# Kernel tuning notes

Hardware: AMD Instinct MI355X
Metric: run time of the kernel (lower is better)

## Reference

```python
import jax, jax.numpy as jnp
import numpy as np

B, N, C, L = 32, 1024, 128, 4

def setup_inputs() -> dict:
    key = jax.random.key(0)
    ks = jax.random.split(key, 8)
    x = jax.random.normal(ks[0], (B, N, C), dtype=jnp.float32)
    # binary adjacency: nonzero entries become unit-weight edges (edge weights unused in module)
    adj = jax.random.randint(ks[1], (B, N, N), 0, 2).astype(jnp.float32)
    mask = jnp.ones((B, N), dtype=jnp.float32)
    s = 1.0 / np.sqrt(C)
    weight = jax.random.uniform(ks[2], (L, C, C), minval=-s, maxval=s, dtype=jnp.float32)
    w_ih = jax.random.uniform(ks[3], (L, 3 * C, C), minval=-s, maxval=s, dtype=jnp.float32)
    w_hh = jax.random.uniform(ks[4], (L, 3 * C, C), minval=-s, maxval=s, dtype=jnp.float32)
    b_ih = jax.random.uniform(ks[5], (L, 3 * C), minval=-s, maxval=s, dtype=jnp.float32)
    b_hh = jax.random.uniform(ks[6], (L, 3 * C), minval=-s, maxval=s, dtype=jnp.float32)
    return {"x": x, "adj": adj, "mask": mask, "weight": weight,
            "w_ih": w_ih, "w_hh": w_hh, "b_ih": b_ih, "b_hh": b_hh}

def _gru_cell(m, h, w_ih, w_hh, b_ih, b_hh):
    # PyTorch GRUCell, gate order (r, z, n)
    gx = m @ w_ih.T + b_ih
    gh = h @ w_hh.T + b_hh
    xr, xz, xn = jnp.split(gx, 3, axis=-1)
    hr, hz, hn = jnp.split(gh, 3, axis=-1)
    r = jax.nn.sigmoid(xr + hr)
    z = jax.nn.sigmoid(xz + hz)
    n = jnp.tanh(xn + r * hn)
    return (1.0 - z) * n + z * h

def reference(x, adj, mask, weight, w_ih, w_hh, b_ih, b_hh):
    h = x  # [B, N, C]; in_channels == out_channels so no zero-padding needed
    for i in range(L):
        hw = jnp.einsum('bnc,cd->bnd', h, weight[i])
        # scatter-add of messages source->target == A^T @ (h W), unit edge weights
        m = jnp.einsum('bjn,bjd->bnd', adj, hw)
        h = _gru_cell(m, h, w_ih[i], w_hh[i], b_ih[i], b_hh[i])
    return h * mask[:, :, None]
```

## Files before the change

kernel.cpp:

```cpp
#include <hip/hip_runtime.h>
#include <stdint.h>


#define NB 32
#define NN 1024
#define NC 128
#define NL 4
#define MTOT (NB * NN)

#define KT 64
#define PITCH 72
#define MP 136

typedef __attribute__((ext_vector_type(8))) short s16x8;
typedef __attribute__((ext_vector_type(4))) float f32x4;
typedef __attribute__((ext_vector_type(2))) unsigned int u32x2;
typedef unsigned short U16;
typedef unsigned int U32;

__device__ __forceinline__ U16 f2bf(float f) {
    union { float f; U32 u; } v; v.f = f;
    return (U16)((v.u + 0x7FFFu + ((v.u >> 16) & 1u)) >> 16);
}
__device__ __forceinline__ float bf2f(U16 h) {
    union { U32 u; float f; } v; v.u = ((U32)h) << 16;
    return v.f;
}
__device__ __forceinline__ void splitbf(float x, U16& hi, U16& lo) {
    hi = f2bf(x);
    lo = f2bf(x - bf2f(hi));
}
__device__ __forceinline__ float sigmoidf_(float x) { return 1.f / (1.f + __expf(-x)); }

__device__ __forceinline__ void glds16(const void* g, void* l) {
    __builtin_amdgcn_global_load_lds(
        (const __attribute__((address_space(1))) void*)g,
        (__attribute__((address_space(3))) void*)l, 16, 0, 0);
}

#define SWZ(row, g) ((row) * 64 + ((((g) ^ ((row) & 7))) * 8))

__global__ __launch_bounds__(256) void k_setup(
    const float* __restrict__ adj, U16* __restrict__ adjT,
    const float* __restrict__ w, const float* __restrict__ wih, const float* __restrict__ whh,
    U16* __restrict__ wThi, U16* __restrict__ wTlo,
    U16* __restrict__ wihhi, U16* __restrict__ wihlo,
    U16* __restrict__ whhhi, U16* __restrict__ whhlo,
    const float* __restrict__ x, U16* __restrict__ hhi, U16* __restrict__ hlo)
{
    __shared__ float t[64 * 65];
    const int bid = blockIdx.x, tid = threadIdx.x;
    if (bid < 8192) {
        const int b = bid >> 8, rem = bid & 255;
        const int j0 = (rem & 15) * 64, n0 = (rem >> 4) * 64;
        const int rr = tid >> 4, c4 = (tid & 15) * 4;
#pragma unroll
        for (int p = 0; p < 4; ++p) {
            int j = p * 16 + rr;
            f32x4 v = *(const f32x4*)&adj[((size_t)b << 20) + ((size_t)(j0 + j) << 10) + n0 + c4];
#pragma unroll
            for (int u = 0; u < 4; ++u) t[j * 65 + c4 + u] = v[u];
        }
        __syncthreads();
#pragma unroll
        for (int p = 0; p < 4; ++p) {
            int n = p * 16 + rr;
            U16 h0 = f2bf(t[(c4 + 0) * 65 + n]);
            U16 h1 = f2bf(t[(c4 + 1) * 65 + n]);
            U16 h2 = f2bf(t[(c4 + 2) * 65 + n]);
            U16 h3 = f2bf(t[(c4 + 3) * 65 + n]);
            u32x2 pk; pk[0] = (U32)h0 | ((U32)h1 << 16); pk[1] = (U32)h2 | ((U32)h3 << 16);
            *(u32x2*)&adjT[((size_t)b << 20) + ((size_t)(n0 + n) << 10) + j0 + c4] = pk;
        }
    } else if (bid < 9984) {
        int i = (bid - 8192) * 256 + tid;
        if (i < 65536) {
            int l = i >> 14, rem = i & 16383, c = rem >> 7, d = rem & 127;
            U16 hi, lo; splitbf(w[i], hi, lo);
            int o = (l << 14) + (d << 7) + c;
            wThi[o] = hi; wTlo[o] = lo;
        } else if (i < 262144) {
            int j = i - 65536;
            U16 hi, lo; splitbf(wih[j], hi, lo);
            wihhi[j] = hi; wihlo[j] = lo;
        } else {
            int j = i - 262144;
            U16 hi, lo; splitbf(whh[j], hi, lo);
            whhhi[j] = hi; whhlo[j] = lo;
        }
    } else {
        int base = (bid - 9984) * 2048 + tid;
#pragma unroll
        for (int p = 0; p < 8; ++p) {
            int i = base + p * 256;
            U16 hi, lo; splitbf(x[i], hi, lo);
            hhi[i] = hi; hlo[i] = lo;
        }
    }
}

struct __align__(16) Smem3 {
    union {
        struct { U16 A[2][128 * PITCH]; U16 B[2][128 * PITCH]; } s;
        float bounce[128 * 129];
    };
};

__global__ __launch_bounds__(256, 2) void k_hw(
    const U16* __restrict__ Ahi, const U16* __restrict__ Alo,
    const U16* __restrict__ Bhi, const U16* __restrict__ Blo,
    U16* __restrict__ Ohi, U16* __restrict__ Olo)
{
    __shared__ Smem3 sm;
    const int tid = threadIdx.x;
    const int lane = tid & 63, wv = tid >> 6;
    const int wr = (wv & 1) * 64, wc = (wv >> 1) * 64;
    const int lm = lane & 15, lk8 = (lane >> 4) * 8;
    const int m0 = blockIdx.x * 128;

    f32x4 acc[4][4] = {};

    for (int kc = 0; kc < 128; kc += KT) {
#pragma unroll
        for (int t = 0; t < 4; ++t) {
            int i = tid + t * 256; int r = i >> 3, v = (i & 7) * 8;
            *(s16x8*)&sm.s.A[0][r * PITCH + v] = *(const s16x8*)&Ahi[(size_t)(m0 + r) * 128 + kc + v];
            *(s16x8*)&sm.s.A[1][r * PITCH + v] = *(const s16x8*)&Alo[(size_t)(m0 + r) * 128 + kc + v];
        }
#pragma unroll
        for (int t = 0; t < 4; ++t) {
            int i = tid + t * 256; int r = i >> 3, v = (i & 7) * 8;
            *(s16x8*)&sm.s.B[0][r * PITCH + v] = *(const s16x8*)&Bhi[r * 128 + kc + v];
            *(s16x8*)&sm.s.B[1][r * PITCH + v] = *(const s16x8*)&Blo[r * 128 + kc + v];
        }
        __syncthreads();
#pragma unroll
        for (int ks = 0; ks < 2; ++ks) {
            const int ko = ks * 32 + lk8;
            s16x8 ahi[4], alo[4], bhi[4], blo[4];
#pragma unroll
            for (int q = 0; q < 4; ++q) {
                ahi[q] = *(const s16x8*)&sm.s.A[0][(wr + q * 16 + lm) * PITCH + ko];
                alo[q] = *(const s16x8*)&sm.s.A[1][(wr + q * 16 + lm) * PITCH + ko];
                bhi[q] = *(const s16x8*)&sm.s.B[0][(wc + q * 16 + lm) * PITCH + ko];
                blo[q] = *(const s16x8*)&sm.s.B[1][(wc + q * 16 + lm) * PITCH + ko];
            }
#pragma unroll
            for (int rt = 0; rt < 4; ++rt)
#pragma unroll
                for (int ct = 0; ct < 4; ++ct) {
                    f32x4 a = acc[rt][ct];
                    a = __builtin_amdgcn_mfma_f32_16x16x32_bf16(ahi[rt], bhi[ct], a, 0, 0, 0);
                    a = __builtin_amdgcn_mfma_f32_16x16x32_bf16(ahi[rt], blo[ct], a, 0, 0, 0);
                    a = __builtin_amdgcn_mfma_f32_16x16x32_bf16(alo[rt], bhi[ct], a, 0, 0, 0);
                    acc[rt][ct] = a;
                }
        }
        __syncthreads();
    }
#pragma unroll
    for (int rt = 0; rt < 4; ++rt)
#pragma unroll
        for (int ct = 0; ct < 4; ++ct)
#pragma unroll
            for (int r = 0; r < 4; ++r)
                sm.bounce[(wr + rt * 16 + (lane >> 4) * 4 + r) * 129 + wc + ct * 16 + lm] = acc[rt][ct][r];
    __syncthreads();
    const int b = m0 >> 10, j0 = m0 & 1023;
    for (int t = 0; t < 32; ++t) {
        int i = tid + t * 256; int d = i >> 6, j2 = (i & 63) * 2;
        float x0 = sm.bounce[j2 * 129 + d], x1 = sm.bounce[(j2 + 1) * 129 + d];
        U16 h0, l0, h1, l1; splitbf(x0, h0, l0); splitbf(x1, h1, l1);
        size_t o = (((size_t)(b * 128 + d)) << 10) + j0 + j2;
        *(U32*)&Ohi[o] = (U32)h0 | ((U32)h1 << 16);
        *(U32*)&Olo[o] = (U32)l0 | ((U32)l1 << 16);
    }
}

__global__ __launch_bounds__(256, 2) void k_mega6(
    const U16* __restrict__ adjT,
    const U16* __restrict__ hwThi, const U16* __restrict__ hwTlo,
    const U16* __restrict__ hhi, const U16* __restrict__ hlo,
    const U16* __restrict__ wihhi, const U16* __restrict__ wihlo,
    const U16* __restrict__ whhhi, const U16* __restrict__ whhlo,
    const float* __restrict__ bih, const float* __restrict__ bhh,
    const float* __restrict__ mask,
    U16* __restrict__ houthi, U16* __restrict__ houtlo,
    float* __restrict__ out, int last)
{
    __shared__ union {
        struct { U16 As[2][64 * 64]; U16 Bh[2][128 * 64]; U16 Bl[2][128 * 64]; } st;
        struct { U16 Mhi[64 * MP]; U16 Mlo[64 * MP]; } m;
    } u;
    const int tid = threadIdx.x;
    const int lane = tid & 63, wv = tid >> 6;
    const int wd0 = wv * 32;
    const int lm = lane & 15, lk8 = (lane >> 4) * 8, quad = lane >> 4;
    const int xcd = blockIdx.x & 7;
    const int j = blockIdx.x >> 3;
    const int bt = xcd * 4 + (j >> 4);
    const int n0 = (j & 15) * 64;
    const int row0 = bt * NN + n0;

#define STAGE(kc, b)                                                                     \
    {                                                                                    \
        _Pragma("unroll")                                                                \
        for (int t = 0; t < 2; ++t) {                                                    \
            int li = tid + t * 256; int r = li >> 3, sg = li & 7;                        \
            glds16(&adjT[((size_t)bt << 20) + ((size_t)(n0 + r) << 10) + (kc)            \
                         + ((sg ^ (r & 7)) * 8)],                                        \
                   &u.st.As[b][li * 8]);                                                 \
        }                                                                                \
        _Pragma("unroll")                                                                \
        for (int t = 0; t < 4; ++t) {                                                    \
            int li = tid + t * 256; int d = li >> 3, sg = li & 7;                        \
            size_t o = (((size_t)(bt * 128 + d)) << 10) + (kc) + ((sg ^ (d & 7)) * 8);   \
            glds16(&hwThi[o], &u.st.Bh[b][li * 8]);                                      \
            glds16(&hwTlo[o], &u.st.Bl[b][li * 8]);                                      \
        }                                                                                \
    }

    f32x4 macc[4][2] = {};
    STAGE(0, 0);
    for (int c = 0; c < 16; ++c) {
        const int b = c & 1;
        __syncthreads();
        if (c + 1 < 16) STAGE((c + 1) * 64, b ^ 1);
#pragma unroll
        for (int ks = 0; ks < 2; ++ks) {
            const int g = ks * 4 + quad;
            s16x8 a[4], bh[2], bl[2];
#pragma unroll
            for (int q = 0; q < 4; ++q)
                a[q] = *(const s16x8*)&u.st.As[b][SWZ(q * 16 + lm, g)];
#pragma unroll
            for (int q = 0; q < 2; ++q) {
                bh[q] = *(const s16x8*)&u.st.Bh[b][SWZ(wd0 + q * 16 + lm, g)];
                bl[q] = *(const s16x8*)&u.st.Bl[b][SWZ(wd0 + q * 16 + lm, g)];
            }
#pragma unroll
            for (int rt = 0; rt < 4; ++rt)
#pragma unroll
                for (int ct = 0; ct < 2; ++ct) {
                    f32x4 cc = macc[rt][ct];
                    cc = __builtin_amdgcn_mfma_f32_16x16x32_bf16(a[rt], bh[ct], cc, 0, 0, 0);
                    cc = __builtin_amdgcn_mfma_f32_16x16x32_bf16(a[rt], bl[ct], cc, 0, 0, 0);
                    macc[rt][ct] = cc;
                }
        }
    }
#undef STAGE
    __syncthreads();

#pragma unroll
    for (int rt = 0; rt < 4; ++rt)
#pragma unroll
        for (int ct = 0; ct < 2; ++ct)
#pragma unroll
            for (int rr = 0; rr < 4; ++rr) {
                int rloc = rt * 16 + quad * 4 + rr;
                int d = wd0 + ct * 16 + lm;
                U16 hi, lo; splitbf(macc[rt][ct][rr], hi, lo);
                u.m.Mhi[rloc * MP + d] = hi;
                u.m.Mlo[rloc * MP + d] = lo;
            }

    f32x4 aR[4][2], aZ[4][2], aXN[4][2], aHN[4][2];
#pragma unroll
    for (int ct = 0; ct < 2; ++ct) {
        const int col = wd0 + ct * 16 + lm;
        const float bR  = bih[col]       + bhh[col];
        const float bZ  = bih[128 + col] + bhh[128 + col];
        const float bXN = bih[256 + col];
        const float bHN = bhh[256 + col];
#pragma unroll
        for (int rt = 0; rt < 4; ++rt) {
            aR[rt][ct]  = f32x4{bR, bR, bR, bR};
            aZ[rt][ct]  = f32x4{bZ, bZ, bZ, bZ};
            aXN[rt][ct] = f32x4{bXN, bXN, bXN, bXN};
            aHN[rt][ct] = f32x4{bHN, bHN, bHN, bHN};
        }
    }

    for (int cc = 0; cc < 4; ++cc) {
        const int ch = (cc + 2) & 3;
        if (cc == 2) __syncthreads();
        const U16* __restrict__ Whi = (ch < 2) ? wihhi : whhhi;
        const U16* __restrict__ Wlo = (ch < 2) ? wihlo : whhlo;
        const int kb = (ch & 1) * 64;
#pragma unroll
        for (int ks = 0; ks < 2; ++ks) {
            const int ko = kb + ks * 32 + lk8;
            s16x8 ahi[4], alo[4];
            if (ch < 2) {
#pragma unroll
                for (int q = 0; q < 4; ++q) {
                    ahi[q] = *(const s16x8*)&u.m.Mhi[(q * 16 + lm) * MP + ko];
                    alo[q] = *(const s16x8*)&u.m.Mlo[(q * 16 + lm) * MP + ko];
                }
            } else {
#pragma unroll
                for (int q = 0; q < 4; ++q) {
                    size_t ao = (size_t)(row0 + q * 16 + lm) * 128 + ko;
                    ahi[q] = *(const s16x8*)&hhi[ao];
                    alo[q] = *(const s16x8*)&hlo[ao];
                }
            }
#pragma unroll
            for (int ct = 0; ct < 2; ++ct) {
                const int col = wd0 + ct * 16 + lm;
                s16x8 bhiR = *(const s16x8*)&Whi[(size_t)col * 128 + ko];
                s16x8 bloR = *(const s16x8*)&Wlo[(size_t)col * 128 + ko];
                s16x8 bhiZ = *(const s16x8*)&Whi[(size_t)(128 + col) * 128 + ko];
                s16x8 bloZ = *(const s16x8*)&Wlo[(size_t)(128 + col) * 128 + ko];
                s16x8 bhiN = *(const s16x8*)&Whi[(size_t)(256 + col) * 128 + ko];
                s16x8 bloN = *(const s16x8*)&Wlo[(size_t)(256 + col) * 128 + ko];
#pragma unroll
                for (int rt = 0; rt < 4; ++rt) {
                    f32x4 r = aR[rt][ct];
                    r = __builtin_amdgcn_mfma_f32_16x16x32_bf16(ahi[rt], bhiR, r, 0, 0, 0);
                    r = __builtin_amdgcn_mfma_f32_16x16x32_bf16(ahi[rt], bloR, r, 0, 0, 0);
                    r = __builtin_amdgcn_mfma_f32_16x16x32_bf16(alo[rt], bhiR, r, 0, 0, 0);
                    aR[rt][ct] = r;
                    f32x4 z = aZ[rt][ct];
                    z = __builtin_amdgcn_mfma_f32_16x16x32_bf16(ahi[rt], bhiZ, z, 0, 0, 0);
                    z = __builtin_amdgcn_mfma_f32_16x16x32_bf16(ahi[rt], bloZ, z, 0, 0, 0);
                    z = __builtin_amdgcn_mfma_f32_16x16x32_bf16(alo[rt], bhiZ, z, 0, 0, 0);
                    aZ[rt][ct] = z;
                }
                if (ch < 2) {
#pragma unroll
                    for (int rt = 0; rt < 4; ++rt) {
                        f32x4 n = aXN[rt][ct];
                        n = __builtin_amdgcn_mfma_f32_16x16x32_bf16(ahi[rt], bhiN, n, 0, 0, 0);
                        n = __builtin_amdgcn_mfma_f32_16x16x32_bf16(ahi[rt], bloN, n, 0, 0, 0);
                        n = __builtin_amdgcn_mfma_f32_16x16x32_bf16(alo[rt], bhiN, n, 0, 0, 0);
                        aXN[rt][ct] = n;
                    }
                } else {
#pragma unroll
                    for (int rt = 0; rt < 4; ++rt) {
                        f32x4 n = aHN[rt][ct];
                        n = __builtin_amdgcn_mfma_f32_16x16x32_bf16(ahi[rt], bhiN, n, 0, 0, 0);
                        n = __builtin_amdgcn_mfma_f32_16x16x32_bf16(ahi[rt], bloN, n, 0, 0, 0);
                        n = __builtin_amdgcn_mfma_f32_16x16x32_bf16(alo[rt], bhiN, n, 0, 0, 0);
                        aHN[rt][ct] = n;
                    }
                }
            }
        }
    }

#pragma unroll
    for (int rt = 0; rt < 4; ++rt) {
#pragma unroll
        for (int ct = 0; ct < 2; ++ct) {
            const int col = wd0 + ct * 16 + lm;
#pragma unroll
            for (int rr = 0; rr < 4; ++rr) {
                const int row = row0 + rt * 16 + quad * 4 + rr;
                float r = sigmoidf_(aR[rt][ct][rr]);
                float z = sigmoidf_(aZ[rt][ct][rr]);
                float n = tanhf(aXN[rt][ct][rr] + r * aHN[rt][ct][rr]);
                size_t ho = (size_t)row * 128 + col;
                float hv = bf2f(hhi[ho]) + bf2f(hlo[ho]);
                float hnew = (1.f - z) * n + z * hv;
                if (last) {
                    out[ho] = hnew * mask[row];
                } else {
                    U16 hi2, lo2; splitbf(hnew, hi2, lo2);
                    houthi[ho] = hi2;
                    houtlo[ho] = lo2;
                }
            }
        }
    }
}

extern "C" void kernel_launch(void* const* d_in, const int* in_sizes, int n_in,
                              void* d_out, int out_size, void* d_ws, size_t ws_size,
                              hipStream_t stream) {
    (void)in_sizes; (void)n_in; (void)out_size; (void)ws_size;
    const float* x    = (const float*)d_in[0];
    const float* adj  = (const float*)d_in[1];
    const float* mask = (const float*)d_in[2];
    const float* wgt  = (const float*)d_in[3];
    const float* wih  = (const float*)d_in[4];
    const float* whh  = (const float*)d_in[5];
    const float* bih  = (const float*)d_in[6];
    const float* bhh  = (const float*)d_in[7];
    float* out = (float*)d_out;

    char* p = (char*)d_ws;
    U16* adjT    = (U16*)p;                p += (size_t)NB * NN * NN * 2;
    U16* h_hi    = (U16*)p;                p += (size_t)MTOT * NC * 2;
    U16* h_lo    = (U16*)p;                p += (size_t)MTOT * NC * 2;
    U16* hwT_hi  = (U16*)p;                p += (size_t)NB * NC * NN * 2;
    U16* hwT_lo  = (U16*)p;                p += (size_t)NB * NC * NN * 2;
    U16* wT_hi   = (U16*)p;                p += (size_t)NL * NC * NC * 2;
    U16* wT_lo   = (U16*)p;                p += (size_t)NL * NC * NC * 2;
    U16* wih_hi  = (U16*)p;                p += (size_t)NL * 384 * NC * 2;
    U16* wih_lo  = (U16*)p;                p += (size_t)NL * 384 * NC * 2;
    U16* whh_hi  = (U16*)p;                p += (size_t)NL * 384 * NC * 2;
    U16* whh_lo  = (U16*)p;                p += (size_t)NL * 384 * NC * 2;

    k_setup<<<12032, 256, 0, stream>>>(adj, adjT, wgt, wih, whh,
                                       wT_hi, wT_lo, wih_hi, wih_lo, whh_hi, whh_lo,
                                       x, h_hi, h_lo);

    for (int l = 0; l < NL; ++l) {
        k_hw<<<256, 256, 0, stream>>>(h_hi, h_lo,
                                      wT_hi + l * 16384, wT_lo + l * 16384,
                                      hwT_hi, hwT_lo);
        k_mega6<<<512, 256, 0, stream>>>(adjT, hwT_hi, hwT_lo, h_hi, h_lo,
                                         wih_hi + l * 49152, wih_lo + l * 49152,
                                         whh_hi + l * 49152, whh_lo + l * 49152,
                                         bih + l * 384, bhh + l * 384, mask,
                                         h_hi, h_lo, out, (l == NL - 1) ? 1 : 0);
    }
}
```

Measured before the change: 514.9 us.

## Retile hW GEMM to 64-row blocks with direct A loads and swizzled async B staging

The h·W kernel now uses 64-row tiles across 512 blocks with higher occupancy (launch bounds 4). The A operand is read straight from global memory into registers instead of being staged in LDS. Only the weight tile B is staged, through global-to-LDS loads with an XOR swizzle. This shrinks LDS usage and should improve occupancy and grid fill, at the cost of uncoalesced direct A reads. The change relies on glds16 and SWZ helpers assumed to be defined elsewhere.

```diff
diff --git a/kernel.cpp b/kernel.cpp
--- a/kernel.cpp
+++ b/kernel.cpp
@@ -8,8 +8,6 @@
 #define NL 4
 #define MTOT (NB * NN)
 
-#define KT 64
-#define PITCH 72
 #define MP 136
 
 typedef __attribute__((ext_vector_type(8))) short s16x8;
@@ -99,56 +97,52 @@
     }
 }
 
-struct __align__(16) Smem3 {
-    union {
-        struct { U16 A[2][128 * PITCH]; U16 B[2][128 * PITCH]; } s;
-        float bounce[128 * 129];
-    };
-};
-
-__global__ __launch_bounds__(256, 2) void k_hw(
+__global__ __launch_bounds__(256, 4) void k_hw2(
     const U16* __restrict__ Ahi, const U16* __restrict__ Alo,
     const U16* __restrict__ Bhi, const U16* __restrict__ Blo,
     U16* __restrict__ Ohi, U16* __restrict__ Olo)
 {
-    __shared__ Smem3 sm;
+    __shared__ union {
+        struct { U16 Bh[128 * 64]; U16 Bl[128 * 64]; } bs;
+        float bounce[64 * 129];
+    } u;
     const int tid = threadIdx.x;
     const int lane = tid & 63, wv = tid >> 6;
-    const int wr = (wv & 1) * 64, wc = (wv >> 1) * 64;
-    const int lm = lane & 15, lk8 = (lane >> 4) * 8;
-    const int m0 = blockIdx.x * 128;
-
-    f32x4 acc[4][4] = {};
-
-    for (int kc = 0; kc < 128; kc += KT) {
+    const int wd0 = wv * 32;
+    const int lm = lane & 15, lk8 = (lane >> 4) * 8, quad = lane >> 4;
+    const int m0 = blockIdx.x * 64;
+
+    f32x4 acc[4][2] = {};
+
+    for (int kc = 0; kc < 128; kc += 64) {
 #pragma unroll
         for (int t = 0; t < 4; ++t) {
-            int i = tid + t * 256; int r = i >> 3, v = (i & 7) * 8;
-            *(s16x8*)&sm.s.A[0][r * PITCH + v] = *(const s16x8*)&Ahi[(size_t)(m0 + r) * 128 + kc + v];
-            *(s16x8*)&sm.s.A[1][r * PITCH + v] = *(const s16x8*)&Alo[(size_t)(m0 + r) * 128 + kc + v];
-        }
-#pragma unroll
-        for (int t = 0; t < 4; ++t) {
-            int i = tid + t * 256; int r = i >> 3, v = (i & 7) * 8;
-            *(s16x8*)&sm.s.B[0][r * PITCH + v] = *(const s16x8*)&Bhi[r * 128 + kc + v];
-            *(s16x8*)&sm.s.B[1][r * PITCH + v] = *(const s16x8*)&Blo[r * 128 + kc + v];
+            int li = tid + t * 256; int d = li >> 3, sg = li & 7;
+            int go = d * 128 + kc + ((sg ^ (d & 7)) * 8);
+            glds16(&Bhi[go], &u.bs.Bh[li * 8]);
+            glds16(&Blo[go], &u.bs.Bl[li * 8]);
         }
         __syncthreads();
 #pragma unroll
         for (int ks = 0; ks < 2; ++ks) {
-            const int ko = ks * 32 + lk8;
-            s16x8 ahi[4], alo[4], bhi[4], blo[4];
+            const int k0 = kc + ks * 32 + lk8;
+            const int g = ks * 4 + quad;
+            s16x8 ahi[4], alo[4], bhi[2], blo[2];
 #pragma unroll
             for (int q = 0; q < 4; ++q) {
-                ahi[q] = *(const s16x8*)&sm.s.A[0][(wr + q * 16 + lm) * PITCH + ko];
-                alo[q] = *(const s16x8*)&sm.s.A[1][(wr + q * 16 + lm) * PITCH + ko];
-                bhi[q] = *(const s16x8*)&sm.s.B[0][(wc + q * 16 + lm) * PITCH + ko];
-                blo[q] = *(const s16x8*)&sm.s.B[1][(wc + q * 16 + lm) * PITCH + ko];
+                size_t ao = (size_t)(m0 + q * 16 + lm) * 128 + k0;
+                ahi[q] = *(const s16x8*)&Ahi[ao];
+                alo[q] = *(const s16x8*)&Alo[ao];
+            }
+#pragma unroll
+            for (int q = 0; q < 2; ++q) {
+                bhi[q] = *(const s16x8*)&u.bs.Bh[SWZ(wd0 + q * 16 + lm, g)];
+                blo[q] = *(const s16x8*)&u.bs.Bl[SWZ(wd0 + q * 16 + lm, g)];
             }
 #pragma unroll
             for (int rt = 0; rt < 4; ++rt)
 #pragma unroll
-                for (int ct = 0; ct < 4; ++ct) {
+                for (int ct = 0; ct < 2; ++ct) {
                     f32x4 a = acc[rt][ct];
                     a = __builtin_amdgcn_mfma_f32_16x16x32_bf16(ahi[rt], bhi[ct], a, 0, 0, 0);
                     a = __builtin_amdgcn_mfma_f32_16x16x32_bf16(ahi[rt], blo[ct], a, 0, 0, 0);
@@ -158,18 +152,20 @@
         }
         __syncthreads();
     }
+
 #pragma unroll
     for (int rt = 0; rt < 4; ++rt)
 #pragma unroll
-        for (int ct = 0; ct < 4; ++ct)
+        for (int ct = 0; ct < 2; ++ct)
 #pragma unroll
             for (int r = 0; r < 4; ++r)
-                sm.bounce[(wr + rt * 16 + (lane >> 4) * 4 + r) * 129 + wc + ct * 16 + lm] = acc[rt][ct][r];
+                u.bounce[(rt * 16 + quad * 4 + r) * 129 + wd0 + ct * 16 + lm] = acc[rt][ct][r];
     __syncthreads();
     const int b = m0 >> 10, j0 = m0 & 1023;
-    for (int t = 0; t < 32; ++t) {
-        int i = tid + t * 256; int d = i >> 6, j2 = (i & 63) * 2;
-        float x0 = sm.bounce[j2 * 129 + d], x1 = sm.bounce[(j2 + 1) * 129 + d];
+#pragma unroll
+    for (int t = 0; t < 16; ++t) {
+        int i = tid + t * 256; int d = i >> 5, j2 = (i & 31) * 2;
+        float x0 = u.bounce[j2 * 129 + d], x1 = u.bounce[(j2 + 1) * 129 + d];
         U16 h0, l0, h1, l1; splitbf(x0, h0, l0); splitbf(x1, h1, l1);
         size_t o = (((size_t)(b * 128 + d)) << 10) + j0 + j2;
         *(U32*)&Ohi[o] = (U32)h0 | ((U32)h1 << 16);
@@ -409,9 +405,9 @@
                                        x, h_hi, h_lo);
 
     for (int l = 0; l < NL; ++l) {
-        k_hw<<<256, 256, 0, stream>>>(h_hi, h_lo,
-                                      wT_hi + l * 16384, wT_lo + l * 16384,
-                                      hwT_hi, hwT_lo);
+        k_hw2<<<512, 256, 0, stream>>>(h_hi, h_lo,
+                                       wT_hi + l * 16384, wT_lo + l * 16384,
+                                       hwT_hi, hwT_lo);
         k_mega6<<<512, 256, 0, stream>>>(adjT, hwT_hi, hwT_lo, h_hi, h_lo,
                                          wih_hi + l * 49152, wih_lo + l * 49152,
                                          whh_hi + l * 49152, whh_lo + l * 49152,
```

Result: no change. 519.7 us (+0.9%).
